# Kernel tuning notes

Measured on AMD Instinct MI355X. Metric: run time of the kernel, lower is better.

## Reference

```python
import jax, jax.numpy as jnp
import numpy as np

DIM = 1024
N_HEAD = 16
HEAD_DIM = DIM // N_HEAD


def setup_inputs() -> dict:
    key = jax.random.key(0)
    ks = jax.random.split(key, 5)
    scale = 0.02
    x = jax.random.normal(ks[0], (4, 2048, DIM), dtype=jnp.float32)
    W_qkv = jax.random.normal(ks[1], (DIM, 3 * DIM), dtype=jnp.float32) * scale
    b_qkv = jnp.zeros((3 * DIM,), dtype=jnp.float32)
    W_proj = jax.random.normal(ks[2], (DIM, DIM), dtype=jnp.float32) * scale
    b_proj = jnp.zeros((DIM,), dtype=jnp.float32)
    return {"x": x, "W_qkv": W_qkv, "b_qkv": b_qkv, "W_proj": W_proj, "b_proj": b_proj}


def reference(x, W_qkv, b_qkv, W_proj, b_proj):
    B, N, C = x.shape
    qkv = x @ W_qkv + b_qkv                       # [B,N,3C]
    qkv = qkv.reshape(B, N, 3, N_HEAD, HEAD_DIM)
    q, k, v = qkv[:, :, 0], qkv[:, :, 1], qkv[:, :, 2]   # [B,N,H,d]
    # scores: [B,H,N,N]
    att = jnp.einsum('bnhd,bmhd->bhnm', q, k) * (1.0 / np.sqrt(HEAD_DIM))
    att = jax.nn.softmax(att, axis=-1)
    out = jnp.einsum('bhnm,bmhd->bnhd', att, v).reshape(B, N, C)
    return out @ W_proj + b_proj
```

## Files before the change

### kernel.cpp

```cpp
#include <hip/hip_runtime.h>
#include <stdint.h>

#define DEV __device__ __forceinline__

typedef __bf16 bf16x8 __attribute__((ext_vector_type(8)));
typedef float f32x4 __attribute__((ext_vector_type(4)));
typedef float f32x16 __attribute__((ext_vector_type(16)));

DEV uint16_t f2bf(float f) {
  union { float f; uint32_t u; } v; v.f = f;
  return (uint16_t)((v.u + 0x7FFFu + ((v.u >> 16) & 1u)) >> 16);
}
DEV float bf2f(uint16_t b) {
  union { uint32_t u; float f; } v; v.u = (uint32_t)b << 16;
  return v.f;
}

#define GLD_LDS(gsrc, ldst)                                                   \
  __builtin_amdgcn_global_load_lds(                                           \
      (__attribute__((address_space(1))) void*)(void*)(gsrc),                 \
      (__attribute__((address_space(3))) void*)(ldst), 16, 0, 0)

__global__ __launch_bounds__(256) void k_conv_x(const float* __restrict__ in,
                                                uint16_t* __restrict__ out,
                                                int n8) {
  int i = blockIdx.x * 256 + threadIdx.x;
  if (i >= n8) return;
  const float4* p = (const float4*)in;
  float4 a = p[i * 2], b = p[i * 2 + 1];
  union { uint16_t s[8]; uint4 v; } o;
  o.s[0] = f2bf(a.x); o.s[1] = f2bf(a.y); o.s[2] = f2bf(a.z); o.s[3] = f2bf(a.w);
  o.s[4] = f2bf(b.x); o.s[5] = f2bf(b.y); o.s[6] = f2bf(b.z); o.s[7] = f2bf(b.w);
  ((uint4*)out)[i] = o.v;
}

__global__ __launch_bounds__(256) void k_transpose_w(const float* __restrict__ in,
                                                     uint16_t* __restrict__ out,
                                                     int K, int Ncols) {
  __shared__ float tile[32][33];
  int n0 = blockIdx.x * 32, k0 = blockIdx.y * 32;
  int tx = threadIdx.x & 31, ty = threadIdx.x >> 5;
  #pragma unroll
  for (int r = ty; r < 32; r += 8)
    tile[r][tx] = in[(size_t)(k0 + r) * Ncols + n0 + tx];
  __syncthreads();
  #pragma unroll
  for (int r = ty; r < 32; r += 8)
    out[(size_t)(n0 + r) * K + k0 + tx] = f2bf(tile[tx][r]);
}

template <int MODE>
__global__ __launch_bounds__(256) void k_gemm(
    const uint16_t* __restrict__ A, const uint16_t* __restrict__ BT,
    const float* __restrict__ bias, float* __restrict__ fout, int Ndim,
    uint16_t* __restrict__ qb, uint16_t* __restrict__ kb,
    uint16_t* __restrict__ vtb) {
  __shared__ uint16_t As[128 * 32];
  __shared__ uint16_t Bs[128 * 32];
  const int K = 1024;
  int tid = threadIdx.x;
  int lane = tid & 63, wid = tid >> 6;
  int lg = lane >> 4, lr = lane & 15;
  int wr = wid >> 1, wc = wid & 1;
  int bm = blockIdx.x, bn = blockIdx.y;

  int c0 = tid, c1 = tid + 256;
  int r0 = c0 >> 2, sl0 = (c0 & 3) ^ (r0 & 3);
  int r1 = c1 >> 2, sl1 = (c1 & 3) ^ (r1 & 3);
  const uint16_t* gA0 = A + (size_t)(bm * 128 + r0) * K + sl0 * 8;
  const uint16_t* gA1 = A + (size_t)(bm * 128 + r1) * K + sl1 * 8;
  const uint16_t* gB0 = BT + (size_t)(bn * 128 + r0) * K + sl0 * 8;
  const uint16_t* gB1 = BT + (size_t)(bn * 128 + r1) * K + sl1 * 8;
  uint16_t* lA0 = &As[(wid * 64) * 8];
  uint16_t* lA1 = &As[(256 + wid * 64) * 8];
  uint16_t* lB0 = &Bs[(wid * 64) * 8];
  uint16_t* lB1 = &Bs[(256 + wid * 64) * 8];

  f32x4 acc[4][4] = {};

  for (int ks = 0; ks < K / 32; ++ks) {
    __syncthreads();
    int ko = ks * 32;
    GLD_LDS(gA0 + ko, lA0);
    GLD_LDS(gA1 + ko, lA1);
    GLD_LDS(gB0 + ko, lB0);
    GLD_LDS(gB1 + ko, lB1);
    __syncthreads();
    bf16x8 af[4], bfv[4];
    #pragma unroll
    for (int i = 0; i < 4; ++i) {
      int row = wr * 64 + i * 16 + lr;
      af[i] = *(const bf16x8*)&As[row * 32 + ((lg ^ (row & 3)) << 3)];
    }
    #pragma unroll
    for (int j = 0; j < 4; ++j) {
      int row = wc * 64 + j * 16 + lr;
      bfv[j] = *(const bf16x8*)&Bs[row * 32 + ((lg ^ (row & 3)) << 3)];
    }
    #pragma unroll
    for (int i = 0; i < 4; ++i)
      #pragma unroll
      for (int j = 0; j < 4; ++j)
        acc[i][j] = __builtin_amdgcn_mfma_f32_16x16x32_bf16(af[i], bfv[j],
                                                            acc[i][j], 0, 0, 0);
  }

  int m0 = bm * 128 + wr * 64;
  int n0 = bn * 128 + wc * 64;
  if (MODE == 1) {
    #pragma unroll
    for (int i = 0; i < 4; ++i) {
      int row = m0 + i * 16 + lg * 4;
      #pragma unroll
      for (int j = 0; j < 4; ++j) {
        int col = n0 + j * 16 + lr;
        float bv = bias[col];
        #pragma unroll
        for (int r = 0; r < 4; ++r)
          fout[(size_t)(row + r) * Ndim + col] = acc[i][j][r] + bv;
      }
    }
  } else {
    #pragma unroll
    for (int i = 0; i < 4; ++i) {
      int rowb = m0 + i * 16 + lg * 4;
      int b = rowb >> 11, t = rowb & 2047;
      #pragma unroll
      for (int j = 0; j < 4; ++j) {
        int colb = n0 + j * 16 + lr;
        int which = colb >> 10;
        int hd = colb & 1023;
        int h = hd >> 6, d = hd & 63;
        float bv = bias[colb];
        size_t bh = (size_t)(b * 16 + h);
        if (which == 2) {
          union { uint16_t s[4]; uint2 v; } pk;
          #pragma unroll
          for (int r = 0; r < 4; ++r) pk.s[r] = f2bf(acc[i][j][r] + bv);
          *(uint2*)&vtb[(bh * 64 + d) * 2048 + t] = pk.v;
        } else {
          uint16_t* dst = which ? kb : qb;
          #pragma unroll
          for (int r = 0; r < 4; ++r)
            dst[(bh * 2048 + t + r) * 64 + d] = f2bf(acc[i][j][r] + bv);
        }
      }
    }
  }
}

__global__ __launch_bounds__(256) void k_attn(const uint16_t* __restrict__ qb,
                                              const uint16_t* __restrict__ kb,
                                              const uint16_t* __restrict__ vtb,
                                              uint16_t* __restrict__ ob) {
  __shared__ uint16_t Ks[64 * 64];
  __shared__ uint16_t Vs[64 * 64];
  int tid = threadIdx.x, lane = tid & 63, wid = tid >> 6;
  int l31 = lane & 31, hi = lane >> 5, x7 = lane & 7;
  int bh = blockIdx.x, qt = blockIdx.y;
  const uint16_t* qbh = qb + (size_t)bh * 2048 * 64;
  const uint16_t* kbh = kb + (size_t)bh * 2048 * 64;
  const uint16_t* vbh = vtb + (size_t)bh * 64 * 2048;
  int q = qt * 128 + wid * 32 + l31;

  const float QSC = 0.18033688011112042f;
  bf16x8 qf[4];
  #pragma unroll
  for (int ks = 0; ks < 4; ++ks) {
    union { uint16_t s[8]; bf16x8 v; uint4 u; } ti, to;
    ti.u = *(const uint4*)(qbh + (size_t)q * 64 + ks * 16 + hi * 8);
    #pragma unroll
    for (int e = 0; e < 8; ++e) to.s[e] = f2bf(bf2f(ti.s[e]) * QSC);
    qf[ks] = to.v;
  }

  f32x16 ovt[2] = {};
  float mrow = -3.0e38f, lrow = 0.f;

  int r0 = tid >> 3, sl0 = (tid & 7) ^ (r0 & 7);
  int r1 = r0 + 32, sl1 = (tid & 7) ^ (r1 & 7);
  uint16_t* lK0 = &Ks[(wid * 64) * 8];
  uint16_t* lK1 = &Ks[(256 + wid * 64) * 8];
  uint16_t* lV0 = &Vs[(wid * 64) * 8];
  uint16_t* lV1 = &Vs[(256 + wid * 64) * 8];

  for (int kt = 0; kt < 32; ++kt) {
    __syncthreads();
    GLD_LDS(kbh + (size_t)(kt * 64 + r0) * 64 + sl0 * 8, lK0);
    GLD_LDS(kbh + (size_t)(kt * 64 + r1) * 64 + sl1 * 8, lK1);
    GLD_LDS(vbh + (size_t)r0 * 2048 + kt * 64 + sl0 * 8, lV0);
    GLD_LDS(vbh + (size_t)r1 * 2048 + kt * 64 + sl1 * 8, lV1);
    __syncthreads();

    f32x16 sv[2] = {};
    __builtin_amdgcn_s_setprio(1);
    #pragma unroll
    for (int kvt = 0; kvt < 2; ++kvt) {
      int row = kvt * 32 + l31;
      #pragma unroll
      for (int ks = 0; ks < 4; ++ks) {
        bf16x8 kf = *(const bf16x8*)&Ks[row * 64 + (((ks * 2 + hi) ^ x7) << 3)];
        sv[kvt] = __builtin_amdgcn_mfma_f32_32x32x16_bf16(kf, qf[ks], sv[kvt], 0, 0, 0);
      }
    }
    __builtin_amdgcn_s_setprio(0);

    float pm = sv[0][0];
    #pragma unroll
    for (int t = 0; t < 2; ++t)
      #pragma unroll
      for (int r = 0; r < 16; ++r) pm = fmaxf(pm, sv[t][r]);
    pm = fmaxf(pm, __shfl_xor(pm, 32));

    if (__any(pm > mrow + 8.f)) {
      float mnew = fmaxf(mrow, pm);
      float alpha = __builtin_amdgcn_exp2f(mrow - mnew);
      mrow = mnew;
      lrow *= alpha;
      #pragma unroll
      for (int t = 0; t < 2; ++t)
        #pragma unroll
        for (int r = 0; r < 16; ++r) ovt[t][r] *= alpha;
    }

    float ps = 0.f;
    #pragma unroll
    for (int t = 0; t < 2; ++t)
      #pragma unroll
      for (int r = 0; r < 16; ++r) {
        float p = __builtin_amdgcn_exp2f(sv[t][r] - mrow);
        sv[t][r] = p;
        ps += p;
      }
    lrow += ps + __shfl_xor(ps, 32);

    union PB { uint32_t w[4]; bf16x8 v; } pb[4];
    #pragma unroll
    for (int t = 0; t < 2; ++t)
      #pragma unroll
      for (int s = 0; s < 2; ++s) {
        int rb = s * 8;
        #pragma unroll
        for (int i = 0; i < 2; ++i) {
          uint32_t a, b;
          asm("v_cvt_pk_bf16_f32 %0, %1, %2"
              : "=v"(a) : "v"(sv[t][rb + 2 * i]), "v"(sv[t][rb + 2 * i + 1]));
          asm("v_cvt_pk_bf16_f32 %0, %1, %2"
              : "=v"(b) : "v"(sv[t][rb + 4 + 2 * i]), "v"(sv[t][rb + 4 + 2 * i + 1]));
          asm("v_permlane32_swap_b32 %0, %1" : "+v"(a), "+v"(b));
          pb[2 * t + s].w[i] = a;
          pb[2 * t + s].w[2 + i] = b;
        }
      }

    __builtin_amdgcn_s_setprio(1);
    #pragma unroll
    for (int dt = 0; dt < 2; ++dt) {
      int row = dt * 32 + l31;
      #pragma unroll
      for (int ks = 0; ks < 4; ++ks) {
        bf16x8 vf = *(const bf16x8*)&Vs[row * 64 + (((ks * 2 + hi) ^ x7) << 3)];
        ovt[dt] = __builtin_amdgcn_mfma_f32_32x32x16_bf16(vf, pb[ks].v, ovt[dt], 0, 0, 0);
      }
    }
    __builtin_amdgcn_s_setprio(0);
  }

  float inv = 1.f / lrow;
  int b = bh >> 4, h = bh & 15;
  size_t base = ((size_t)b * 2048 + q) * 1024 + h * 64;
  #pragma unroll
  for (int dt = 0; dt < 2; ++dt)
    #pragma unroll
    for (int r = 0; r < 16; r += 2) {
      int d = dt * 32 + (r & 3) + 8 * (r >> 2) + 4 * hi;
      uint32_t w = (uint32_t)f2bf(ovt[dt][r] * inv) |
                   ((uint32_t)f2bf(ovt[dt][r + 1] * inv) << 16);
      *(uint32_t*)&ob[base + d] = w;
    }
}

extern "C" void kernel_launch(void* const* d_in, const int* in_sizes, int n_in,
                              void* d_out, int out_size, void* d_ws,
                              size_t ws_size, hipStream_t stream) {
  const float* x = (const float*)d_in[0];
  const float* Wqkv = (const float*)d_in[1];
  const float* bqkv = (const float*)d_in[2];
  const float* Wproj = (const float*)d_in[3];
  const float* bproj = (const float*)d_in[4];
  float* out = (float*)d_out;
  char* ws = (char*)d_ws;

  uint16_t* xb = (uint16_t*)(ws);
  uint16_t* wqkvt = (uint16_t*)(ws + (16ull << 20));
  uint16_t* wprojt = (uint16_t*)(ws + (22ull << 20));
  uint16_t* qbuf = (uint16_t*)(ws + (24ull << 20));
  uint16_t* kbuf = (uint16_t*)(ws + (40ull << 20));
  uint16_t* vtb = (uint16_t*)(ws + (56ull << 20));
  uint16_t* ob = xb;

  k_conv_x<<<4096, 256, 0, stream>>>(x, xb, 1048576);
  k_transpose_w<<<dim3(96, 32), 256, 0, stream>>>(Wqkv, wqkvt, 1024, 3072);
  k_transpose_w<<<dim3(32, 32), 256, 0, stream>>>(Wproj, wprojt, 1024, 1024);
  k_gemm<0><<<dim3(64, 24), 256, 0, stream>>>(xb, wqkvt, bqkv, nullptr, 3072,
                                              qbuf, kbuf, vtb);
  k_attn<<<dim3(64, 16), 256, 0, stream>>>(qbuf, kbuf, vtb, ob);
  k_gemm<1><<<dim3(64, 8), 256, 0, stream>>>(ob, wprojt, bproj, out, 1024,
                                             nullptr, nullptr, nullptr);
}
```

Before: 234.2 us.

## Double-buffer K/V tiles in attention, change LDS swizzle and block ordering

```diff
diff --git a/kernel.cpp b/kernel.cpp
--- a/kernel.cpp
+++ b/kernel.cpp
@@ -153,11 +153,14 @@
                                               const uint16_t* __restrict__ kb,
                                               const uint16_t* __restrict__ vtb,
                                               uint16_t* __restrict__ ob) {
-  __shared__ uint16_t Ks[64 * 64];
-  __shared__ uint16_t Vs[64 * 64];
+  __shared__ uint16_t Ks[2][64 * 64];
+  __shared__ uint16_t Vs[2][64 * 64];
   int tid = threadIdx.x, lane = tid & 63, wid = tid >> 6;
-  int l31 = lane & 31, hi = lane >> 5, x7 = lane & 7;
-  int bh = blockIdx.x, qt = blockIdx.y;
+  int l31 = lane & 31, hi = lane >> 5;
+  int rx = (l31 & 7) ^ (((l31 >> 3) & 3) << 1);
+  int bid = blockIdx.x;
+  int bh = (bid & 7) * 8 + ((bid >> 3) & 7);
+  int qt = bid >> 6;
   const uint16_t* qbh = qb + (size_t)bh * 2048 * 64;
   const uint16_t* kbh = kb + (size_t)bh * 2048 * 64;
   const uint16_t* vbh = vtb + (size_t)bh * 64 * 2048;
@@ -177,20 +180,20 @@
   f32x16 ovt[2] = {};
   float mrow = -3.0e38f, lrow = 0.f;
 
-  int r0 = tid >> 3, sl0 = (tid & 7) ^ (r0 & 7);
-  int r1 = r0 + 32, sl1 = (tid & 7) ^ (r1 & 7);
-  uint16_t* lK0 = &Ks[(wid * 64) * 8];
-  uint16_t* lK1 = &Ks[(256 + wid * 64) * 8];
-  uint16_t* lV0 = &Vs[(wid * 64) * 8];
-  uint16_t* lV1 = &Vs[(256 + wid * 64) * 8];
-
-  for (int kt = 0; kt < 32; ++kt) {
-    __syncthreads();
-    GLD_LDS(kbh + (size_t)(kt * 64 + r0) * 64 + sl0 * 8, lK0);
-    GLD_LDS(kbh + (size_t)(kt * 64 + r1) * 64 + sl1 * 8, lK1);
-    GLD_LDS(vbh + (size_t)r0 * 2048 + kt * 64 + sl0 * 8, lV0);
-    GLD_LDS(vbh + (size_t)r1 * 2048 + kt * 64 + sl1 * 8, lV1);
-    __syncthreads();
+  int r0 = tid >> 3;
+  int sx = (tid & 7) ^ (r0 & 7) ^ (((r0 >> 3) & 3) << 1);
+  int r1 = r0 + 32;
+
+  auto stage = [&](int kt, uint16_t* KN, uint16_t* VN) {
+    GLD_LDS(kbh + (size_t)(kt * 64 + r0) * 64 + sx * 8, KN + wid * 512);
+    GLD_LDS(kbh + (size_t)(kt * 64 + r1) * 64 + sx * 8, KN + 2048 + wid * 512);
+    GLD_LDS(vbh + (size_t)r0 * 2048 + kt * 64 + sx * 8, VN + wid * 512);
+    GLD_LDS(vbh + (size_t)r1 * 2048 + kt * 64 + sx * 8, VN + 2048 + wid * 512);
+  };
+
+  auto iter = [&](const uint16_t* KC, const uint16_t* VC, uint16_t* KN,
+                  uint16_t* VN, int ktn, bool dostage, bool dobar) {
+    if (dostage) stage(ktn, KN, VN);
 
     f32x16 sv[2] = {};
     __builtin_amdgcn_s_setprio(1);
@@ -199,7 +202,7 @@
       int row = kvt * 32 + l31;
       #pragma unroll
       for (int ks = 0; ks < 4; ++ks) {
-        bf16x8 kf = *(const bf16x8*)&Ks[row * 64 + (((ks * 2 + hi) ^ x7) << 3)];
+        bf16x8 kf = *(const bf16x8*)&KC[row * 64 + (((ks * 2 + hi) ^ rx) << 3)];
         sv[kvt] = __builtin_amdgcn_mfma_f32_32x32x16_bf16(kf, qf[ks], sv[kvt], 0, 0, 0);
       }
     }
@@ -259,11 +262,25 @@
       int row = dt * 32 + l31;
       #pragma unroll
       for (int ks = 0; ks < 4; ++ks) {
-        bf16x8 vf = *(const bf16x8*)&Vs[row * 64 + (((ks * 2 + hi) ^ x7) << 3)];
+        bf16x8 vf = *(const bf16x8*)&VC[row * 64 + (((ks * 2 + hi) ^ rx) << 3)];
         ovt[dt] = __builtin_amdgcn_mfma_f32_32x32x16_bf16(vf, pb[ks].v, ovt[dt], 0, 0, 0);
       }
     }
     __builtin_amdgcn_s_setprio(0);
+
+    if (dobar) {
+      asm volatile("s_waitcnt vmcnt(0)" ::: "memory");
+      __syncthreads();
+    }
+  };
+
+  stage(0, Ks[0], Vs[0]);
+  asm volatile("s_waitcnt vmcnt(0)" ::: "memory");
+  __syncthreads();
+
+  for (int t = 0; t < 32; t += 2) {
+    iter(Ks[0], Vs[0], Ks[1], Vs[1], t + 1, true, true);
+    iter(Ks[1], Vs[1], Ks[0], Vs[0], t + 2, t + 2 < 32, t + 2 < 32);
   }
 
   float inv = 1.f / lrow;
@@ -304,7 +321,7 @@
   k_transpose_w<<<dim3(32, 32), 256, 0, stream>>>(Wproj, wprojt, 1024, 1024);
   k_gemm<0><<<dim3(64, 24), 256, 0, stream>>>(xb, wqkvt, bqkv, nullptr, 3072,
                                               qbuf, kbuf, vtb);
-  k_attn<<<dim3(64, 16), 256, 0, stream>>>(qbuf, kbuf, vtb, ob);
+  k_attn<<<1024, 256, 0, stream>>>(qbuf, kbuf, vtb, ob);
   k_gemm<1><<<dim3(64, 8), 256, 0, stream>>>(ob, wprojt, bproj, out, 1024,
                                              nullptr, nullptr, nullptr);
 }
```

New measurement: 213.0 us. -9.0%, faster.
